# Optimization experiments

Measured on AMD Instinct MI355X. Metric: run time of the kernel, lower is better.

Reference implementation:

```python
import jax, jax.numpy as jnp
import numpy as np

SCALE = 16.0  # hard-coded divisor in the original module (implies head_dim 256)


def setup_inputs() -> dict:
    key = jax.random.key(0)
    kq, kk, kv = jax.random.split(key, 3)
    B, H, S, D = 4, 8, 2048, 256
    return {
        "queries": jax.random.normal(kq, (B, H, S, D), dtype=jnp.float32),
        "keys": jax.random.normal(kk, (B, H, S, D), dtype=jnp.float32),
        "values": jax.random.normal(kv, (B, H, S, D), dtype=jnp.float32),
        "adj": jnp.ones((S, S), dtype=jnp.int32),  # unused (dead code in original)
    }


def reference(queries, keys, values, adj):
    # scores: [B, H, S, S]
    scores = jnp.einsum("bhqd,bhkd->bhqk", queries, keys) / SCALE
    attn = jax.nn.softmax(scores, axis=-1)
    h = jnp.einsum("bhqk,bhkd->bhqd", attn, values)  # [B, H, S, D]
    B, H, S, D = h.shape
    # original uses .view(S, B, H, D) on the contiguous output: a raw reshape
    return jnp.reshape(h, (S, B, H, D))
```

## Files before the change

### kernel.cpp

```cpp
#include <hip/hip_runtime.h>

#define S_LEN 2048
#define D_DIM 256
#define NBH   32
#define BM    64
#define BN    64
#define NKT   32
#define TILE_ELS 16384
#define WS_NEED  67108864ull

typedef float    float4v __attribute__((ext_vector_type(4)));
typedef short    short8  __attribute__((ext_vector_type(8)));
typedef unsigned uint4v  __attribute__((ext_vector_type(4)));
typedef __bf16   bf16x8  __attribute__((ext_vector_type(8)));
typedef __bf16   bf16x2  __attribute__((ext_vector_type(2)));
typedef __bf16   bf16x4  __attribute__((ext_vector_type(4)));

#define QSCALE (0.0625f * 1.44269504088896340736f)
#define NEG_BIG (-3.0e38f)

typedef __attribute__((address_space(1))) const void gv_t;
typedef __attribute__((address_space(3))) void lv_t;

__global__ __launch_bounds__(256) void prep_k(const float* __restrict__ Kg,
                                              __bf16* __restrict__ kimg) {
    const int gi = blockIdx.x * 256 + threadIdx.x;
    const int c  = gi & 31;
    const int sg = gi >> 5;
    const int s  = sg & 2047;
    const int kt = s >> 6;
    const int sr = s & 63;
    const int bh = sg >> 11;
    const float* src = Kg + ((size_t)sg << 8) + (c << 3);
    const float4v a = *(const float4v*)src;
    const float4v b = *(const float4v*)(src + 4);
    bf16x8 w;
    w[0]=(__bf16)a[0]; w[1]=(__bf16)a[1]; w[2]=(__bf16)a[2]; w[3]=(__bf16)a[3];
    w[4]=(__bf16)b[0]; w[5]=(__bf16)b[1]; w[6]=(__bf16)b[2]; w[7]=(__bf16)b[3];
    const int cp = c ^ (sr & 7);
    *(bf16x8*)(kimg + ((size_t)(bh * NKT + kt) << 14) + sr * 256 + cp * 8) = w;
}

__global__ __launch_bounds__(256) void prep_v(const float* __restrict__ Vg,
                                              __bf16* __restrict__ vimg) {
    __shared__ __bf16 t[64 * 258];
    const int tid = threadIdx.x;
    const int blk = blockIdx.x;
    const float* src = Vg + ((size_t)blk << 14);
    #pragma unroll 4
    for (int i = 0; i < 16; ++i) {
        const int g = i * 256 + tid;
        const int s = g >> 6;
        const int d = (g & 63) << 2;
        const float4v v = *(const float4v*)(src + s * 256 + d);
        __bf16* p = &t[s * 258 + d];
        *(bf16x2*)p       = (bf16x2){(__bf16)v[0], (__bf16)v[1]};
        *(bf16x2*)(p + 2) = (bf16x2){(__bf16)v[2], (__bf16)v[3]};
    }
    __syncthreads();
    __bf16* dst = vimg + ((size_t)blk << 14);
    #pragma unroll 2
    for (int i = 0; i < 8; ++i) {
        const int d = i * 32 + (tid >> 3);
        const int c = tid & 7;
        bf16x8 w;
        #pragma unroll
        for (int k = 0; k < 8; ++k) w[k] = t[(c * 8 + k) * 258 + d];
        const int cp = c ^ (d & 7);
        *(bf16x8*)(dst + d * 64 + cp * 8) = w;
    }
}

__device__ __forceinline__ void dma8(const char* g, char* l) {
    #pragma unroll
    for (int i = 0; i < 8; ++i)
        __builtin_amdgcn_global_load_lds((gv_t*)(g + i * 1024), (lv_t*)(l + i * 1024), 16, 0, 0);
}

__device__ __forceinline__ int pack_bf16(float a, float b) {
    const unsigned short ua = __builtin_bit_cast(unsigned short, (__bf16)a);
    const unsigned short ub = __builtin_bit_cast(unsigned short, (__bf16)b);
    return (int)((unsigned)ua | ((unsigned)ub << 16));
}

__global__ __launch_bounds__(256, 2)
void fa_main(const float* __restrict__ Qg, const __bf16* __restrict__ kimg,
             const __bf16* __restrict__ vimg, float* __restrict__ Og) {
    __shared__ __bf16 Kbuf[64 * 256];
    __shared__ __bf16 Vbuf[256 * 64];

    const int tid  = threadIdx.x;
    const int wave = tid >> 6;
    const int lane = tid & 63;
    const int n16  = lane & 15;
    const int quad = lane >> 4;
    const int n167 = n16 & 7;

    const int linear = blockIdx.x;
    const int bh = ((linear & 7) << 2) + (linear >> 8);
    const int qt = (linear >> 3) & 31;

    const size_t base = (size_t)bh * (S_LEN * D_DIM);
    const char* ktile = (const char*)(kimg + ((size_t)bh << 19));
    const char* vtile = (const char*)(vimg + ((size_t)bh << 19));
    const int woff = wave * 8192 + lane * 16;
    char* kl = (char*)Kbuf + wave * 8192;
    char* vl = (char*)Vbuf + wave * 8192;

    short8 qfrag[8];
    {
        const float* qrow = Qg + base + (size_t)(qt * BM + wave * 16 + n16) * D_DIM;
        #pragma unroll
        for (int kk = 0; kk < 8; ++kk) {
            const float4v a = *(const float4v*)(qrow + kk * 32 + quad * 8);
            const float4v b = *(const float4v*)(qrow + kk * 32 + quad * 8 + 4);
            short8 f;
            f[0] = __builtin_bit_cast(short, (__bf16)(a[0] * QSCALE));
            f[1] = __builtin_bit_cast(short, (__bf16)(a[1] * QSCALE));
            f[2] = __builtin_bit_cast(short, (__bf16)(a[2] * QSCALE));
            f[3] = __builtin_bit_cast(short, (__bf16)(a[3] * QSCALE));
            f[4] = __builtin_bit_cast(short, (__bf16)(b[0] * QSCALE));
            f[5] = __builtin_bit_cast(short, (__bf16)(b[1] * QSCALE));
            f[6] = __builtin_bit_cast(short, (__bf16)(b[2] * QSCALE));
            f[7] = __builtin_bit_cast(short, (__bf16)(b[3] * QSCALE));
            qfrag[kk] = f;
        }
    }

    float4v oacc[16];
    #pragma unroll
    for (int i = 0; i < 16; ++i) oacc[i] = (float4v){0.f, 0.f, 0.f, 0.f};
    float m_run = NEG_BIG, l_run = 0.f;

    dma8(ktile + woff, kl);
    dma8(vtile + woff, vl);

    const int srcA = n16 + ((lane & 16) << 1);
    const int srcB = srcA + 16;
    const bool hi  = (quad >> 1) != 0;

    for (int kt = 0; kt < NKT; ++kt) {
        __syncthreads();
        if (kt > 0) dma8(vtile + kt * 32768 + woff, vl);

        float4v sacc[4];
        #pragma unroll
        for (int nt = 0; nt < 4; ++nt) {
            float4v acc = {0.f, 0.f, 0.f, 0.f};
            const __bf16* kp = &Kbuf[(nt * 16 + n16) * 256];
            #pragma unroll
            for (int kk = 0; kk < 8; ++kk) {
                const short8 kfrag = *(const short8*)(kp + (((4 * kk + quad) ^ n167) << 3));
                acc = __builtin_amdgcn_mfma_f32_16x16x32_bf16(kfrag, qfrag[kk], acc, 0, 0, 0);
            }
            sacc[nt] = acc;
        }

        float mx = sacc[0][0];
        #pragma unroll
        for (int nt = 0; nt < 4; ++nt)
            #pragma unroll
            for (int r = 0; r < 4; ++r) mx = fmaxf(mx, sacc[nt][r]);
        mx = fmaxf(mx, __shfl_xor(mx, 16));
        mx = fmaxf(mx, __shfl_xor(mx, 32));
        const float mn = fmaxf(m_run, mx);
        const float al = exp2f(m_run - mn);
        m_run = mn;

        float ps = 0.f;
        int pk[4][2];
        #pragma unroll
        for (int nt = 0; nt < 4; ++nt) {
            float p0 = exp2f(sacc[nt][0] - mn);
            float p1 = exp2f(sacc[nt][1] - mn);
            float p2 = exp2f(sacc[nt][2] - mn);
            float p3 = exp2f(sacc[nt][3] - mn);
            ps += (p0 + p1) + (p2 + p3);
            pk[nt][0] = pack_bf16(p0, p1);
            pk[nt][1] = pack_bf16(p2, p3);
        }
        ps += __shfl_xor(ps, 16);
        ps += __shfl_xor(ps, 32);
        l_run = l_run * al + ps;

        #pragma unroll
        for (int r = 0; r < 4; ++r) {
            const float alr = __shfl(al, (quad << 4) + (quad << 2) + r);
            #pragma unroll
            for (int dt = 0; dt < 16; ++dt) oacc[dt][r] *= alr;
        }

        __syncthreads();
        if (kt < NKT - 1) dma8(ktile + (kt + 1) * 32768 + woff, kl);

        short8 pfrag[2];
        #pragma unroll
        for (int kth = 0; kth < 2; ++kth) {
            const int a0 = __shfl(pk[2 * kth][0], srcA), a1 = __shfl(pk[2 * kth + 1][0], srcA);
            const int b0 = __shfl(pk[2 * kth][1], srcA), b1 = __shfl(pk[2 * kth + 1][1], srcA);
            const int c0 = __shfl(pk[2 * kth][0], srcB), c1 = __shfl(pk[2 * kth + 1][0], srcB);
            const int d0 = __shfl(pk[2 * kth][1], srcB), d1 = __shfl(pk[2 * kth + 1][1], srcB);
            uint4v u;
            u[0] = (unsigned)(hi ? a1 : a0);
            u[1] = (unsigned)(hi ? b1 : b0);
            u[2] = (unsigned)(hi ? c1 : c0);
            u[3] = (unsigned)(hi ? d1 : d0);
            pfrag[kth] = __builtin_bit_cast(short8, u);
        }

        #pragma unroll
        for (int kth = 0; kth < 2; ++kth) {
            #pragma unroll
            for (int dt = 0; dt < 16; ++dt) {
                const short8 vfrag = *(const short8*)
                    &Vbuf[(dt * 16 + n16) * 64 + (((4 * kth + quad) ^ n167) << 3)];
                oacc[dt] = __builtin_amdgcn_mfma_f32_16x16x32_bf16(pfrag[kth], vfrag, oacc[dt], 0, 0, 0);
            }
        }
    }

    float* obase = Og + base + (size_t)(qt * BM + wave * 16) * D_DIM;
    #pragma unroll
    for (int r = 0; r < 4; ++r) {
        const float lr  = __shfl(l_run, (quad << 4) + (quad << 2) + r);
        const float inv = 1.0f / lr;
        const int row = (quad << 2) + r;
        #pragma unroll
        for (int dt = 0; dt < 16; ++dt)
            obase[row * D_DIM + dt * 16 + n16] = oacc[dt][r] * inv;
    }
}

__global__ __launch_bounds__(256, 3)
void fa_fallback(const float* __restrict__ Qg, const float* __restrict__ Kg,
                 const float* __restrict__ Vg, float* __restrict__ Og)
{
    __shared__ __bf16 kv[256 * 72];
    __shared__ __bf16 pbuf[4 * 16 * 72];
    const int tid = threadIdx.x, wave = tid >> 6, lane = tid & 63;
    const int n16 = lane & 15, quad = lane >> 4;
    const int linear = blockIdx.x;
    const int bh = ((linear & 7) << 2) + (linear >> 8);
    const int qt = (linear >> 3) & 31;
    const size_t base = (size_t)bh * S_LEN * D_DIM;
    short8 qfrag[8];
    {
        const float* qrow = Qg + base + (size_t)(qt * BM + wave * 16 + n16) * D_DIM;
        #pragma unroll
        for (int kk = 0; kk < 8; ++kk) {
            const float4v a = *(const float4v*)(qrow + kk * 32 + quad * 8);
            const float4v b = *(const float4v*)(qrow + kk * 32 + quad * 8 + 4);
            short8 f;
            f[0] = __builtin_bit_cast(short, (__bf16)(a[0] * QSCALE));
            f[1] = __builtin_bit_cast(short, (__bf16)(a[1] * QSCALE));
            f[2] = __builtin_bit_cast(short, (__bf16)(a[2] * QSCALE));
            f[3] = __builtin_bit_cast(short, (__bf16)(a[3] * QSCALE));
            f[4] = __builtin_bit_cast(short, (__bf16)(b[0] * QSCALE));
            f[5] = __builtin_bit_cast(short, (__bf16)(b[1] * QSCALE));
            f[6] = __builtin_bit_cast(short, (__bf16)(b[2] * QSCALE));
            f[7] = __builtin_bit_cast(short, (__bf16)(b[3] * QSCALE));
            qfrag[kk] = f;
        }
    }
    float4v oacc[16];
    #pragma unroll
    for (int i = 0; i < 16; ++i) oacc[i] = (float4v){0.f, 0.f, 0.f, 0.f};
    float m_run[4] = {NEG_BIG, NEG_BIG, NEG_BIG, NEG_BIG};
    float l_run[4] = {0.f, 0.f, 0.f, 0.f};
    for (int kt = 0; kt < S_LEN / BN; ++kt) {
        {
            const float* kbase = Kg + base + (size_t)kt * BN * D_DIM;
            #pragma unroll 4
            for (int it = 0; it < 16; ++it) {
                const int g = it * 256 + tid;
                const int row = g >> 6;
                const int dc = (g & 63) << 2;
                const float4v v = *(const float4v*)(kbase + row * D_DIM + dc);
                bf16x4 w;
                w[0] = (__bf16)v[0]; w[1] = (__bf16)v[1];
                w[2] = (__bf16)v[2]; w[3] = (__bf16)v[3];
                *(bf16x4*)&kv[row * 264 + dc] = w;
            }
        }
        __syncthreads();
        float4v sacc[4];
        #pragma unroll
        for (int nt = 0; nt < 4; ++nt) {
            float4v acc = {0.f, 0.f, 0.f, 0.f};
            const __bf16* kp = &kv[(nt * 16 + n16) * 264 + quad * 8];
            #pragma unroll
            for (int kk = 0; kk < 8; ++kk) {
                const short8 bfr = *(const short8*)(kp + kk * 32);
                acc = __builtin_amdgcn_mfma_f32_16x16x32_bf16(qfrag[kk], bfr, acc, 0, 0, 0);
            }
            sacc[nt] = acc;
        }
        __syncthreads();
        {
            const float* vbase = Vg + base + (size_t)kt * BN * D_DIM;
            #pragma unroll 4
            for (int it = 0; it < 8; ++it) {
                const int tsk = it * 256 + tid;
                const int kp2 = tsk >> 6;
                const int dc = (tsk & 63) << 2;
                const float4v v0 = *(const float4v*)(vbase + (2 * kp2) * D_DIM + dc);
                const float4v v1 = *(const float4v*)(vbase + (2 * kp2 + 1) * D_DIM + dc);
                #pragma unroll
                for (int i = 0; i < 4; ++i) {
                    bf16x2 w; w[0] = (__bf16)v0[i]; w[1] = (__bf16)v1[i];
                    *(bf16x2*)&kv[(dc + i) * 72 + 2 * kp2] = w;
                }
            }
        }
        #pragma unroll
        for (int r = 0; r < 4; ++r) {
            float mx = fmaxf(fmaxf(sacc[0][r], sacc[1][r]), fmaxf(sacc[2][r], sacc[3][r]));
            mx = fmaxf(mx, __shfl_xor(mx, 1));
            mx = fmaxf(mx, __shfl_xor(mx, 2));
            mx = fmaxf(mx, __shfl_xor(mx, 4));
            mx = fmaxf(mx, __shfl_xor(mx, 8));
            const float mn = fmaxf(m_run[r], mx);
            const float al = exp2f(m_run[r] - mn);
            m_run[r] = mn;
            float ps = 0.f;
            __bf16* prow = &pbuf[wave * 1152 + (quad * 4 + r) * 72 + n16];
            #pragma unroll
            for (int nt = 0; nt < 4; ++nt) {
                const float p = exp2f(sacc[nt][r] - mn);
                ps += p;
                prow[nt * 16] = (__bf16)p;
            }
            ps += __shfl_xor(ps, 1);
            ps += __shfl_xor(ps, 2);
            ps += __shfl_xor(ps, 4);
            ps += __shfl_xor(ps, 8);
            l_run[r] = l_run[r] * al + ps;
            #pragma unroll
            for (int dt = 0; dt < 16; ++dt) oacc[dt][r] *= al;
        }
        __syncthreads();
        #pragma unroll
        for (int kth = 0; kth < 2; ++kth) {
            const short8 af = *(const short8*)&pbuf[wave * 1152 + n16 * 72 + kth * 32 + quad * 8];
            #pragma unroll
            for (int dt = 0; dt < 16; ++dt) {
                const short8 bfr = *(const short8*)&kv[(dt * 16 + n16) * 72 + kth * 32 + quad * 8];
                oacc[dt] = __builtin_amdgcn_mfma_f32_16x16x32_bf16(af, bfr, oacc[dt], 0, 0, 0);
            }
        }
        __syncthreads();
    }
    float* obase = Og + base + (size_t)(qt * BM + wave * 16) * D_DIM;
    #pragma unroll
    for (int r = 0; r < 4; ++r) {
        const float inv = 1.0f / l_run[r];
        const int row = quad * 4 + r;
        #pragma unroll
        for (int dt = 0; dt < 16; ++dt)
            obase[row * D_DIM + dt * 16 + n16] = oacc[dt][r] * inv;
    }
}

extern "C" void kernel_launch(void* const* d_in, const int* in_sizes, int n_in,
                              void* d_out, int out_size, void* d_ws, size_t ws_size,
                              hipStream_t stream) {
    const float* Q = (const float*)d_in[0];
    const float* K = (const float*)d_in[1];
    const float* V = (const float*)d_in[2];
    float* O = (float*)d_out;
    (void)in_sizes; (void)n_in; (void)out_size;
    if (ws_size >= WS_NEED) {
        __bf16* kimg = (__bf16*)d_ws;
        __bf16* vimg = kimg + (size_t)NBH * NKT * TILE_ELS;
        prep_k<<<dim3(8192), dim3(256), 0, stream>>>(K, kimg);
        prep_v<<<dim3(1024), dim3(256), 0, stream>>>(V, vimg);
        fa_main<<<dim3(1024), dim3(256), 0, stream>>>(Q, kimg, vimg, O);
    } else {
        fa_fallback<<<dim3(1024), dim3(256), 0, stream>>>(Q, K, V, O);
    }
}
```

Measured before the change: 436.9 us.

## Double-buffer K/V tiles with 8-wave 128-row query blocks and skip unit rescale

The main attention kernel now runs 512 threads per block, covering 128 query rows, so each K/V tile loaded into LDS is shared by twice as many waves. K and V tiles are double-buffered, with the next tile's async global-to-LDS copy issued at the top of each iteration, which removes one barrier per step. The output-accumulator rescale is skipped when no lane's running max changed. Costs: 128KB of LDS per block, which limits residency to about one block per CU, and only 512 blocks in the grid.

```diff
diff --git a/kernel.cpp b/kernel.cpp
--- a/kernel.cpp
+++ b/kernel.cpp
@@ -3,7 +3,7 @@
 #define S_LEN 2048
 #define D_DIM 256
 #define NBH   32
-#define BM    64
+#define BM    128
 #define BN    64
 #define NKT   32
 #define TILE_ELS 16384
@@ -71,9 +71,9 @@
     }
 }
 
-__device__ __forceinline__ void dma8(const char* g, char* l) {
-    #pragma unroll
-    for (int i = 0; i < 8; ++i)
+__device__ __forceinline__ void dma4(const char* g, char* l) {
+    #pragma unroll
+    for (int i = 0; i < 4; ++i)
         __builtin_amdgcn_global_load_lds((gv_t*)(g + i * 1024), (lv_t*)(l + i * 1024), 16, 0, 0);
 }
 
@@ -83,11 +83,11 @@
     return (int)((unsigned)ua | ((unsigned)ub << 16));
 }
 
-__global__ __launch_bounds__(256, 2)
+__global__ __launch_bounds__(512, 2)
 void fa_main(const float* __restrict__ Qg, const __bf16* __restrict__ kimg,
              const __bf16* __restrict__ vimg, float* __restrict__ Og) {
-    __shared__ __bf16 Kbuf[64 * 256];
-    __shared__ __bf16 Vbuf[256 * 64];
+    __shared__ __bf16 Kbuf[2][64 * 256];
+    __shared__ __bf16 Vbuf[2][256 * 64];
 
     const int tid  = threadIdx.x;
     const int wave = tid >> 6;
@@ -97,15 +97,14 @@
     const int n167 = n16 & 7;
 
     const int linear = blockIdx.x;
-    const int bh = ((linear & 7) << 2) + (linear >> 8);
-    const int qt = (linear >> 3) & 31;
+    const int bh = ((linear & 7) << 2) + (linear >> 7);
+    const int qt = (linear >> 3) & 15;
 
     const size_t base = (size_t)bh * (S_LEN * D_DIM);
     const char* ktile = (const char*)(kimg + ((size_t)bh << 19));
     const char* vtile = (const char*)(vimg + ((size_t)bh << 19));
-    const int woff = wave * 8192 + lane * 16;
-    char* kl = (char*)Kbuf + wave * 8192;
-    char* vl = (char*)Vbuf + wave * 8192;
+    const int woff = wave * 4096 + lane * 16;
+    const int ldso = wave * 4096;
 
     short8 qfrag[8];
     {
@@ -132,22 +131,26 @@
     for (int i = 0; i < 16; ++i) oacc[i] = (float4v){0.f, 0.f, 0.f, 0.f};
     float m_run = NEG_BIG, l_run = 0.f;
 
-    dma8(ktile + woff, kl);
-    dma8(vtile + woff, vl);
+    dma4(ktile + woff, (char*)&Kbuf[0][0] + ldso);
+    dma4(vtile + woff, (char*)&Vbuf[0][0] + ldso);
 
     const int srcA = n16 + ((lane & 16) << 1);
     const int srcB = srcA + 16;
     const bool hi  = (quad >> 1) != 0;
 
     for (int kt = 0; kt < NKT; ++kt) {
-        __syncthreads();
-        if (kt > 0) dma8(vtile + kt * 32768 + woff, vl);
+        const int p = kt & 1;
+        __syncthreads();
+        if (kt + 1 < NKT) {
+            dma4(ktile + (kt + 1) * 32768 + woff, (char*)&Kbuf[1 - p][0] + ldso);
+            dma4(vtile + (kt + 1) * 32768 + woff, (char*)&Vbuf[1 - p][0] + ldso);
+        }
 
         float4v sacc[4];
         #pragma unroll
         for (int nt = 0; nt < 4; ++nt) {
             float4v acc = {0.f, 0.f, 0.f, 0.f};
-            const __bf16* kp = &Kbuf[(nt * 16 + n16) * 256];
+            const __bf16* kp = &Kbuf[p][(nt * 16 + n16) * 256];
             #pragma unroll
             for (int kk = 0; kk < 8; ++kk) {
                 const short8 kfrag = *(const short8*)(kp + (((4 * kk + quad) ^ n167) << 3));
@@ -183,15 +186,14 @@
         ps += __shfl_xor(ps, 32);
         l_run = l_run * al + ps;
 
-        #pragma unroll
-        for (int r = 0; r < 4; ++r) {
-            const float alr = __shfl(al, (quad << 4) + (quad << 2) + r);
-            #pragma unroll
-            for (int dt = 0; dt < 16; ++dt) oacc[dt][r] *= alr;
-        }
-
-        __syncthreads();
-        if (kt < NKT - 1) dma8(ktile + (kt + 1) * 32768 + woff, kl);
+        if (__ballot(al != 1.0f)) {
+            #pragma unroll
+            for (int r = 0; r < 4; ++r) {
+                const float alr = __shfl(al, 20 * quad + r);
+                #pragma unroll
+                for (int dt = 0; dt < 16; ++dt) oacc[dt][r] *= alr;
+            }
+        }
 
         short8 pfrag[2];
         #pragma unroll
@@ -213,7 +215,7 @@
             #pragma unroll
             for (int dt = 0; dt < 16; ++dt) {
                 const short8 vfrag = *(const short8*)
-                    &Vbuf[(dt * 16 + n16) * 64 + (((4 * kth + quad) ^ n167) << 3)];
+                    &Vbuf[p][(dt * 16 + n16) * 64 + (((4 * kth + quad) ^ n167) << 3)];
                 oacc[dt] = __builtin_amdgcn_mfma_f32_16x16x32_bf16(pfrag[kth], vfrag, oacc[dt], 0, 0, 0);
             }
         }
@@ -222,7 +224,7 @@
     float* obase = Og + base + (size_t)(qt * BM + wave * 16) * D_DIM;
     #pragma unroll
     for (int r = 0; r < 4; ++r) {
-        const float lr  = __shfl(l_run, (quad << 4) + (quad << 2) + r);
+        const float lr  = __shfl(l_run, 20 * quad + r);
         const float inv = 1.0f / lr;
         const int row = (quad << 2) + r;
         #pragma unroll
@@ -245,7 +247,7 @@
     const size_t base = (size_t)bh * S_LEN * D_DIM;
     short8 qfrag[8];
     {
-        const float* qrow = Qg + base + (size_t)(qt * BM + wave * 16 + n16) * D_DIM;
+        const float* qrow = Qg + base + (size_t)(qt * 64 + wave * 16 + n16) * D_DIM;
         #pragma unroll
         for (int kk = 0; kk < 8; ++kk) {
             const float4v a = *(const float4v*)(qrow + kk * 32 + quad * 8);
@@ -350,7 +352,7 @@
         }
         __syncthreads();
     }
-    float* obase = Og + base + (size_t)(qt * BM + wave * 16) * D_DIM;
+    float* obase = Og + base + (size_t)(qt * 64 + wave * 16) * D_DIM;
     #pragma unroll
     for (int r = 0; r < 4; ++r) {
         const float inv = 1.0f / l_run[r];
@@ -374,7 +376,7 @@
         __bf16* vimg = kimg + (size_t)NBH * NKT * TILE_ELS;
         prep_k<<<dim3(8192), dim3(256), 0, stream>>>(K, kimg);
         prep_v<<<dim3(1024), dim3(256), 0, stream>>>(V, vimg);
-        fa_main<<<dim3(1024), dim3(256), 0, stream>>>(Q, kimg, vimg, O);
+        fa_main<<<dim3(512), dim3(512), 0, stream>>>(Q, kimg, vimg, O);
     } else {
         fa_fallback<<<dim3(1024), dim3(256), 0, stream>>>(Q, K, V, O);
     }
```

New measurement: 436.1 us. Within noise of the previous version (-0.2%).
